# Kernel optimization log

Hardware: AMD Instinct MI355X
Metric: run time of the kernel (lower is better)

## Reference

```python
import jax, jax.numpy as jnp
import numpy as np

EPS = 1e-5


def gather_nodes(nodes, idx):
    # nodes: [B,N,C], idx: [B,N,K] -> [B,N,K,C]
    return jax.vmap(lambda n, e: n[e])(nodes, idx)


def layer_norm(x, g, b):
    m = jnp.mean(x, axis=-1, keepdims=True)
    v = jnp.mean((x - m) ** 2, axis=-1, keepdims=True)
    return (x - m) * jax.lax.rsqrt(v + EPS) * g + b


def linear(x, W, b):
    return x @ W + b


def setup_inputs() -> dict:
    key = jax.random.key(0)
    B, N, K, H = 2, 2048, 48, 128
    ks = jax.random.split(key, 32)
    it = iter(range(32))
    def nrm(shape, scale=0.05):
        return jax.random.normal(ks[next(it)], shape, dtype=jnp.float32) * scale
    inp = {
        "h_V": nrm((B, N, H), 1.0),
        "h_V_atom": nrm((B, N, H), 1.0),
        "h_E": nrm((B, N, K, H), 1.0),
        # message MLP 1: in = H + 2*(H+H) = 5H = 640
        "W1": nrm((5 * H, H)), "b1": jnp.zeros((H,), jnp.float32),
        "W2": nrm((H, H)), "b2": jnp.zeros((H,), jnp.float32),
        "W3": nrm((H, H)), "b3": jnp.zeros((H,), jnp.float32),
        # message MLP 2: in = H + (H+H) = 3H = 384
        "W11": nrm((3 * H, H)), "b11": jnp.zeros((H,), jnp.float32),
        "W12": nrm((H, H)), "b12": jnp.zeros((H,), jnp.float32),
        "W13": nrm((H, H)), "b13": jnp.zeros((H,), jnp.float32),
        # FFN
        "W_in": nrm((H, 4 * H)), "b_in": jnp.zeros((4 * H,), jnp.float32),
        "W_out": nrm((4 * H, H)), "b_out": jnp.zeros((H,), jnp.float32),
        # LayerNorms
        "g1": jnp.ones((H,), jnp.float32), "be1": jnp.zeros((H,), jnp.float32),
        "g2": jnp.ones((H,), jnp.float32), "be2": jnp.zeros((H,), jnp.float32),
        "g3": jnp.ones((H,), jnp.float32), "be3": jnp.zeros((H,), jnp.float32),
        "mask_V": jnp.ones((B, N), jnp.float32),
        "mask_attend": jnp.ones((B, N, K), jnp.float32),
        "E_idx": jax.random.randint(ks[next(it)], (B, N, K), 0, N),
    }
    return inp


def reference(h_V, h_V_atom, h_E, W1, b1, W2, b2, W3, b3, W11, b11, W12, b12,
              W13, b13, W_in, b_in, W_out, b_out, g1, be1, g2, be2, g3, be3,
              mask_V, mask_attend, E_idx):
    gelu = lambda x: jax.nn.gelu(x, approximate=False)
    SCALE = 30.0
    K = h_E.shape[-2]

    # --- node message ---
    h_EV = jnp.concatenate([
        jnp.broadcast_to(h_V[:, :, None, :], h_E.shape[:3] + (h_V.shape[-1],)),
        h_E, gather_nodes(h_V, E_idx),
        h_E, gather_nodes(h_V_atom, E_idx),
    ], axis=-1)  # [B,N,K,5H]
    h_message = linear(gelu(linear(gelu(linear(h_EV, W1, b1)), W2, b2)), W3, b3)
    h_message = mask_attend[..., None] * h_message
    dh = jnp.sum(h_message, axis=-2) / SCALE
    h_V = layer_norm(h_V + dh, g1, be1)

    # --- FFN ---
    dh = linear(gelu(linear(h_V, W_in, b_in)), W_out, b_out)
    h_V = layer_norm(h_V + dh, g2, be2)
    h_V = mask_V[..., None] * h_V

    # --- edge update ---
    h_EV2 = jnp.concatenate([
        jnp.broadcast_to(h_V[:, :, None, :], h_E.shape[:3] + (h_V.shape[-1],)),
        h_E, gather_nodes(h_V, E_idx),
    ], axis=-1)  # [B,N,K,3H]
    h_message = linear(gelu(linear(gelu(linear(h_EV2, W11, b11)), W12, b12)), W13, b13)
    h_E = layer_norm(h_E + h_message, g3, be3)
    return (h_V, h_E)
```

## Files before the change

### kernel.cpp

```cpp
#include <hip/hip_runtime.h>
#include <hip/hip_bf16.h>

#define H 128
#define NN 2048
#define BB 2
#define EPSF 1e-5f

typedef __bf16 bf16;
typedef bf16 bf16x8 __attribute__((ext_vector_type(8)));
typedef bf16 bf16x4 __attribute__((ext_vector_type(4)));
typedef float f32x4 __attribute__((ext_vector_type(4)));

#define U1_F     155648
#define U2_F     679936
#define HVMID_F  1204224
#define V2_F     1990656
#define V1_F     2252800
#define HVMID_B  3457024

__device__ __forceinline__ float gelu_f(float x) {
    float u = x * x;
    float p = __builtin_fmaf(u, 0.044715f, 1.0f);
    float w = x * p;
    float e = __builtin_amdgcn_exp2f(w * -2.3022083f);
    return x * __builtin_amdgcn_rcpf(1.0f + e);
}

#define MFMA16(a, b, c) __builtin_amdgcn_mfma_f32_16x16x32_bf16((a), (b), (c), 0, 0, 0)

#define GEMM_PIPE(U, A_EXPR, B0p, B1p, ACC)                                       \
    {                                                                             \
        bf16x8 bq0[3], bq1[3];                                                    \
        _Pragma("unroll")                                                         \
        for (int j = 0; j < 3 && j < (U); ++j) {                                  \
            bq0[j] = *(const bf16x8*)((B0p) + j * 32);                            \
            bq1[j] = *(const bf16x8*)((B1p) + j * 32);                            \
        }                                                                         \
        bf16x8 afc[3], afn[3];                                                    \
        _Pragma("unroll")                                                         \
        for (int rt = 0; rt < 3; ++rt) { const int u = 0; afc[rt] = (A_EXPR); }   \
        _Pragma("unroll")                                                         \
        for (int uu = 0; uu < (U); ++uu) {                                        \
            if (uu + 1 < (U)) {                                                   \
                _Pragma("unroll")                                                 \
                for (int rt = 0; rt < 3; ++rt) { const int u = uu + 1; afn[rt] = (A_EXPR); } \
            }                                                                     \
            __builtin_amdgcn_s_setprio(1);                                        \
            _Pragma("unroll")                                                     \
            for (int rt = 0; rt < 3; ++rt) {                                      \
                ACC[rt][0] = MFMA16(afc[rt], bq0[uu % 3], ACC[rt][0]);            \
                ACC[rt][1] = MFMA16(afc[rt], bq1[uu % 3], ACC[rt][1]);            \
            }                                                                     \
            __builtin_amdgcn_s_setprio(0);                                        \
            if (uu + 3 < (U)) {                                                   \
                bq0[uu % 3] = *(const bf16x8*)((B0p) + (uu + 3) * 32);            \
                bq1[uu % 3] = *(const bf16x8*)((B1p) + (uu + 3) * 32);            \
            }                                                                     \
            _Pragma("unroll")                                                     \
            for (int rt = 0; rt < 3; ++rt) afc[rt] = afn[rt];                     \
        }                                                                         \
    }

#define PACK_STORE(DST, ROW, PCOL, V0, V1)                                        \
    {                                                                             \
        union { bf16 h[2]; unsigned u; } pk_;                                     \
        pk_.h[0] = (V0); pk_.h[1] = (V1);                                         \
        *(unsigned*)&DST[ROW][PCOL] = pk_.u;                                      \
    }

__global__ void prep_weights(const float* __restrict__ W1, const float* __restrict__ W2,
                             const float* __restrict__ W3, const float* __restrict__ W11,
                             const float* __restrict__ W12, const float* __restrict__ W13,
                             const float* __restrict__ Win, const float* __restrict__ Wout,
                             bf16* __restrict__ ws)
{
    int i = blockIdx.x * 256 + threadIdx.x;
    float v;
    if (i < 65536) {
        int c = i >> 9, k = i & 511, s = k >> 7, k0 = k & 127;
        if (s == 0)      v = W1[k0 * H + c];
        else if (s == 1) v = W1[(128 + k0) * H + c] + W1[(384 + k0) * H + c];
        else if (s == 2) v = W1[(256 + k0) * H + c];
        else             v = W1[(512 + k0) * H + c];
    } else if (i < 81920)  { int j = i - 65536;  int c = j >> 7, p = j & 127;
                             int k = (p & ~31) + ((p & 1) << 4) + ((p & 31) >> 1);
                             v = W2[k * H + c]; }
    else if (i < 98304)    { int j = i - 81920;  int c = j >> 7, p = j & 127;
                             int k = (p & ~31) + ((p & 1) << 4) + ((p & 31) >> 1);
                             v = W3[k * H + c]; }
    else if (i < 147456)   { int j = i - 98304;  int c = j / 384, k = j - c * 384; v = W11[k * H + c]; }
    else if (i < 163840)   { int j = i - 147456; int c = j >> 7, p = j & 127;
                             int k = (p & ~31) + ((p & 1) << 4) + ((p & 31) >> 1);
                             v = W12[k * H + c]; }
    else if (i < 180224)   { int j = i - 163840; int c = j >> 7, p = j & 127;
                             int k = (p & ~31) + ((p & 1) << 4) + ((p & 31) >> 1);
                             v = W13[k * H + c]; }
    else if (i < 245760)   { int j = i - 180224; int jj = j >> 7, k = j & 127; v = Win[k * 512 + jj]; }
    else                   { int j = i - 245760; int c = j >> 9, k = j & 511; v = Wout[k * H + c]; }
    ws[i] = (bf16)v;
}

__global__ __launch_bounds__(512) void u1_kernel(
    const float* __restrict__ hV, const float* __restrict__ hVa,
    const float* __restrict__ b1, const bf16* __restrict__ ws, float* __restrict__ wsf)
{
    int n0 = blockIdx.x * 128;
    int t = threadIdx.x, w = t >> 6, l = t & 63, l16 = l & 15, lg = l >> 4;
    int wm = w >> 2, wn = w & 3;
    __shared__ __align__(16) bf16 sA[128][136];
    __shared__ __align__(16) bf16 sB[128][136];

    #pragma unroll
    for (int i = 0; i < 8; ++i) {
        int idx = t + i * 512;
        int row = idx >> 5, c4 = (idx & 31) << 2;
        f32x4 v = *(const f32x4*)(hV + (size_t)(n0 + row) * H + c4);
        bf16x4 o; o[0] = (bf16)v[0]; o[1] = (bf16)v[1]; o[2] = (bf16)v[2]; o[3] = (bf16)v[3];
        *(bf16x4*)(&sA[row][c4]) = o;
        f32x4 va = *(const f32x4*)(hVa + (size_t)(n0 + row) * H + c4);
        bf16x4 oa; oa[0] = (bf16)va[0]; oa[1] = (bf16)va[1]; oa[2] = (bf16)va[2]; oa[3] = (bf16)va[3];
        *(bf16x4*)(&sB[row][c4]) = oa;
    }
    __syncthreads();

    f32x4 accU[4][2], accV[4][2];
    #pragma unroll
    for (int rt = 0; rt < 4; ++rt)
        #pragma unroll
        for (int c2 = 0; c2 < 2; ++c2) {
            accU[rt][c2] = (f32x4){0.f, 0.f, 0.f, 0.f};
            accV[rt][c2] = (f32x4){0.f, 0.f, 0.f, 0.f};
        }
    #pragma unroll
    for (int kk = 0; kk < 4; ++kk) {
        bf16x8 af[4];
        #pragma unroll
        for (int rt = 0; rt < 4; ++rt)
            af[rt] = *(const bf16x8*)(&sA[wm * 64 + rt * 16 + l16][kk * 32 + lg * 8]);
        #pragma unroll
        for (int c2 = 0; c2 < 2; ++c2) {
            int c = wn * 32 + c2 * 16 + l16;
            bf16x8 bU = *(const bf16x8*)(&ws[(size_t)c * 512 + kk * 32 + lg * 8]);
            bf16x8 bV = *(const bf16x8*)(&ws[(size_t)c * 512 + 256 + kk * 32 + lg * 8]);
            #pragma unroll
            for (int rt = 0; rt < 4; ++rt) {
                accU[rt][c2] = MFMA16(af[rt], bU, accU[rt][c2]);
                accV[rt][c2] = MFMA16(af[rt], bV, accV[rt][c2]);
            }
        }
    }
    #pragma unroll
    for (int kk = 0; kk < 4; ++kk) {
        bf16x8 af[4];
        #pragma unroll
        for (int rt = 0; rt < 4; ++rt)
            af[rt] = *(const bf16x8*)(&sB[wm * 64 + rt * 16 + l16][kk * 32 + lg * 8]);
        #pragma unroll
        for (int c2 = 0; c2 < 2; ++c2) {
            int c = wn * 32 + c2 * 16 + l16;
            bf16x8 bV = *(const bf16x8*)(&ws[(size_t)c * 512 + 384 + kk * 32 + lg * 8]);
            #pragma unroll
            for (int rt = 0; rt < 4; ++rt)
                accV[rt][c2] = MFMA16(af[rt], bV, accV[rt][c2]);
        }
    }
    #pragma unroll
    for (int c2 = 0; c2 < 2; ++c2) {
        int col = wn * 32 + c2 * 16 + l16;
        float bb = b1[col];
        #pragma unroll
        for (int rt = 0; rt < 4; ++rt)
            #pragma unroll
            for (int i = 0; i < 4; ++i) {
                int row = wm * 64 + rt * 16 + lg * 4 + i;
                wsf[U1_F + (size_t)(n0 + row) * H + col] = accU[rt][c2][i] + bb;
                wsf[V1_F + (size_t)(n0 + row) * H + col] = accV[rt][c2][i];
            }
    }
}

__global__ __launch_bounds__(256, 4) void node_msg_kernel(
    const float* __restrict__ hV, const float* __restrict__ hE,
    const float* __restrict__ b2, const float* __restrict__ b3,
    const float* __restrict__ g1, const float* __restrict__ be1,
    const float* __restrict__ maskA, const int* __restrict__ Eidx,
    bf16* __restrict__ ws, float* __restrict__ wsf)
{
    __shared__ __align__(16) char smem[27136];
    bf16 (*sA)[136]  = (bf16(*)[136])smem;
    bf16 (*sH1)[136] = (bf16(*)[136])smem;
    bf16 (*sH2)[136] = (bf16(*)[136])(smem + 13056);
    float* sDH = (float*)(smem + 26112);

    int n = blockIdx.x, b = n >> 11;
    int t = threadIdx.x, w = t >> 6, l = t & 63, l16 = l & 15, lg = l >> 4;

    int col0 = w * 32 + l16, col1 = col0 + 16;
    int pcol = w * 32 + l16 * 2;
    float u1v0 = wsf[U1_F + (size_t)n * H + col0];
    float u1v1 = wsf[U1_F + (size_t)n * H + col1];
    float b2v0 = b2[col0], b2v1 = b2[col1];
    float b3v0 = b3[col0], b3v1 = b3[col1];

    float v1v0[3][4], v1v1[3][4];
    #pragma unroll
    for (int rt = 0; rt < 3; ++rt)
        #pragma unroll
        for (int i = 0; i < 4; ++i) {
            int row = rt * 16 + lg * 4 + i;
            int nbr = Eidx[n * 48 + row];
            const float* vp = wsf + V1_F + ((size_t)b * NN + nbr) * H;
            v1v0[rt][i] = vp[col0];
            v1v1[rt][i] = vp[col1];
        }

    #pragma unroll
    for (int i = 0; i < 6; ++i) {
        int idx = t + i * 256;
        int row = idx >> 5, c4 = (idx & 31) << 2;
        f32x4 v = *(const f32x4*)(hE + ((size_t)n * 48 + row) * H + c4);
        bf16x4 o; o[0] = (bf16)v[0]; o[1] = (bf16)v[1]; o[2] = (bf16)v[2]; o[3] = (bf16)v[3];
        *(bf16x4*)(&sA[row][c4]) = o;
    }
    __syncthreads();

    f32x4 acc[3][2];
    #pragma unroll
    for (int rt = 0; rt < 3; ++rt)
        #pragma unroll
        for (int c2 = 0; c2 < 2; ++c2) acc[rt][c2] = (f32x4){0.f, 0.f, 0.f, 0.f};
    {
        const bf16* B0 = ws + (size_t)col0 * 512 + 128 + lg * 8;
        const bf16* B1 = ws + (size_t)col1 * 512 + 128 + lg * 8;
        GEMM_PIPE(4, (*(const bf16x8*)(&sA[rt * 16 + l16][u * 32 + lg * 8])), B0, B1, acc)
    }
    __syncthreads();

    #pragma unroll
    for (int rt = 0; rt < 3; ++rt)
        #pragma unroll
        for (int i = 0; i < 4; ++i) {
            int row = rt * 16 + lg * 4 + i;
            bf16 v0 = (bf16)gelu_f(acc[rt][0][i] + u1v0 + v1v0[rt][i]);
            bf16 v1 = (bf16)gelu_f(acc[rt][1][i] + u1v1 + v1v1[rt][i]);
            PACK_STORE(sH1, row, pcol, v0, v1)
        }
    __syncthreads();

    f32x4 a2[3][2];
    #pragma unroll
    for (int rt = 0; rt < 3; ++rt)
        #pragma unroll
        for (int c2 = 0; c2 < 2; ++c2) a2[rt][c2] = (f32x4){0.f, 0.f, 0.f, 0.f};
    {
        const bf16* B0 = ws + 65536 + (size_t)col0 * 128 + lg * 8;
        const bf16* B1 = ws + 65536 + (size_t)col1 * 128 + lg * 8;
        GEMM_PIPE(4, (*(const bf16x8*)(&sH1[rt * 16 + l16][u * 32 + lg * 8])), B0, B1, a2)
    }
    #pragma unroll
    for (int rt = 0; rt < 3; ++rt)
        #pragma unroll
        for (int i = 0; i < 4; ++i) {
            int row = rt * 16 + lg * 4 + i;
            bf16 v0 = (bf16)gelu_f(a2[rt][0][i] + b2v0);
            bf16 v1 = (bf16)gelu_f(a2[rt][1][i] + b2v1);
            PACK_STORE(sH2, row, pcol, v0, v1)
        }
    __syncthreads();

    float mk[3][4];
    #pragma unroll
    for (int rt = 0; rt < 3; ++rt)
        #pragma unroll
        for (int i = 0; i < 4; ++i)
            mk[rt][i] = maskA[n * 48 + rt * 16 + lg * 4 + i];

    f32x4 a3[3][2];
    #pragma unroll
    for (int rt = 0; rt < 3; ++rt)
        #pragma unroll
        for (int c2 = 0; c2 < 2; ++c2) a3[rt][c2] = (f32x4){0.f, 0.f, 0.f, 0.f};
    {
        const bf16* B0 = ws + 81920 + (size_t)col0 * 128 + lg * 8;
        const bf16* B1 = ws + 81920 + (size_t)col1 * 128 + lg * 8;
        GEMM_PIPE(4, (*(const bf16x8*)(&sH2[rt * 16 + l16][u * 32 + lg * 8])), B0, B1, a3)
    }
    float r0s = 0.f, r1s = 0.f;
    #pragma unroll
    for (int rt = 0; rt < 3; ++rt)
        #pragma unroll
        for (int i = 0; i < 4; ++i) {
            r0s += (a3[rt][0][i] + b3v0) * mk[rt][i];
            r1s += (a3[rt][1][i] + b3v1) * mk[rt][i];
        }
    r0s += __shfl_xor(r0s, 16); r0s += __shfl_xor(r0s, 32);
    r1s += __shfl_xor(r1s, 16); r1s += __shfl_xor(r1s, 32);
    if (l < 16) { sDH[w * 32 + l] = r0s; sDH[w * 32 + 16 + l] = r1s; }
    __syncthreads();

    if (w == 0) {
        float x0 = hV[(size_t)n * H + l] + sDH[l] * (1.0f / 30.0f);
        float x1 = hV[(size_t)n * H + l + 64] + sDH[l + 64] * (1.0f / 30.0f);
        float s1 = x0 + x1, s2 = x0 * x0 + x1 * x1;
        #pragma unroll
        for (int off = 32; off; off >>= 1) { s1 += __shfl_xor(s1, off); s2 += __shfl_xor(s2, off); }
        float m = s1 * (1.f / 128.f);
        float rs = rsqrtf(s2 * (1.f / 128.f) - m * m + EPSF);
        float y0 = (x0 - m) * rs * g1[l] + be1[l];
        float y1 = (x1 - m) * rs * g1[l + 64] + be1[l + 64];
        wsf[HVMID_F + (size_t)n * H + l] = y0;
        wsf[HVMID_F + (size_t)n * H + l + 64] = y1;
        ws[HVMID_B + (size_t)n * H + l] = (bf16)y0;
        ws[HVMID_B + (size_t)n * H + l + 64] = (bf16)y1;
    }
}

__global__ __launch_bounds__(512) void ffn_kernel(
    const float* __restrict__ b_in, const float* __restrict__ b_out,
    const float* __restrict__ b11, const float* __restrict__ g2,
    const float* __restrict__ be2, const float* __restrict__ maskV,
    bf16* __restrict__ ws, float* __restrict__ wsf, float* __restrict__ outV)
{
    int n0 = blockIdx.x * 32;
    int t = threadIdx.x, w = t >> 6, l = t & 63, l16 = l & 15, lg = l >> 4;

    __shared__ __align__(16) char smem[8704 + 33280];
    bf16 (*sA)[136]  = (bf16(*)[136])(smem);
    bf16 (*sFF)[520] = (bf16(*)[520])(smem + 8704);
    float (*sX)[132] = (float(*)[132])(smem + 8704);

    {
        int row = t >> 4, c8 = (t & 15) << 3;
        *(bf16x8*)(&sA[row][c8]) = *(const bf16x8*)(ws + HVMID_B + (size_t)(n0 + row) * H + c8);
    }
    __syncthreads();

    f32x4 a1[2][4];
    #pragma unroll
    for (int rt = 0; rt < 2; ++rt)
        #pragma unroll
        for (int ct = 0; ct < 4; ++ct) a1[rt][ct] = (f32x4){0.f, 0.f, 0.f, 0.f};
    #pragma unroll
    for (int kk = 0; kk < 4; ++kk) {
        bf16x8 af[2];
        #pragma unroll
        for (int rt = 0; rt < 2; ++rt)
            af[rt] = *(const bf16x8*)(&sA[rt * 16 + l16][kk * 32 + lg * 8]);
        #pragma unroll
        for (int ct = 0; ct < 4; ++ct) {
            int c = w * 64 + ct * 16 + l16;
            bf16x8 bfr = *(const bf16x8*)(&ws[180224 + (size_t)c * 128 + kk * 32 + lg * 8]);
            #pragma unroll
            for (int rt = 0; rt < 2; ++rt)
                a1[rt][ct] = MFMA16(af[rt], bfr, a1[rt][ct]);
        }
    }
    #pragma unroll
    for (int ct = 0; ct < 4; ++ct) {
        int c = w * 64 + ct * 16 + l16;
        float bb = b_in[c];
        #pragma unroll
        for (int rt = 0; rt < 2; ++rt)
            #pragma unroll
            for (int i = 0; i < 4; ++i) {
                int row = rt * 16 + lg * 4 + i;
                sFF[row][c] = (bf16)gelu_f(a1[rt][ct][i] + bb);
            }
    }
    __syncthreads();

    f32x4 a2[2];
    a2[0] = (f32x4){0.f, 0.f, 0.f, 0.f}; a2[1] = (f32x4){0.f, 0.f, 0.f, 0.f};
    int cc = w * 16 + l16;
    #pragma unroll
    for (int kk = 0; kk < 16; ++kk) {
        bf16x8 af[2];
        #pragma unroll
        for (int rt = 0; rt < 2; ++rt)
            af[rt] = *(const bf16x8*)(&sFF[rt * 16 + l16][kk * 32 + lg * 8]);
        bf16x8 bfr = *(const bf16x8*)(&ws[245760 + (size_t)cc * 512 + kk * 32 + lg * 8]);
        #pragma unroll
        for (int rt = 0; rt < 2; ++rt)
            a2[rt] = MFMA16(af[rt], bfr, a2[rt]);
    }
    __syncthreads();
    {
        float bb = b_out[cc];
        #pragma unroll
        for (int rt = 0; rt < 2; ++rt)
            #pragma unroll
            for (int i = 0; i < 4; ++i) {
                int row = rt * 16 + lg * 4 + i;
                sX[row][cc] = a2[rt][i] + bb + wsf[HVMID_F + (size_t)(n0 + row) * H + cc];
            }
    }
    __syncthreads();

    if (t < 128) {
        int row = t >> 2, q = t & 3;
        float xr[32], s1 = 0.f, s2 = 0.f;
        #pragma unroll
        for (int j = 0; j < 32; ++j) {
            float x = sX[row][q * 32 + j];
            xr[j] = x; s1 += x; s2 += x * x;
        }
        s1 += __shfl_xor(s1, 1); s1 += __shfl_xor(s1, 2);
        s2 += __shfl_xor(s2, 1); s2 += __shfl_xor(s2, 2);
        float m = s1 * (1.f / 128.f);
        float vv = s2 * (1.f / 128.f) - m * m;
        float rs = rsqrtf(vv + EPSF);
        float mv = maskV[n0 + row];
        #pragma unroll
        for (int j = 0; j < 32; ++j) {
            int c = q * 32 + j;
            float y = ((xr[j] - m) * rs * g2[c] + be2[c]) * mv;
            outV[(size_t)(n0 + row) * H + c] = y;
            sA[row][c] = (bf16)y;
        }
    }
    __syncthreads();

    f32x4 a3[2], a4[2];
    a3[0] = (f32x4){0.f, 0.f, 0.f, 0.f}; a3[1] = (f32x4){0.f, 0.f, 0.f, 0.f};
    a4[0] = (f32x4){0.f, 0.f, 0.f, 0.f}; a4[1] = (f32x4){0.f, 0.f, 0.f, 0.f};
    #pragma unroll
    for (int kk = 0; kk < 4; ++kk) {
        bf16x8 af[2];
        #pragma unroll
        for (int rt = 0; rt < 2; ++rt)
            af[rt] = *(const bf16x8*)(&sA[rt * 16 + l16][kk * 32 + lg * 8]);
        bf16x8 bU = *(const bf16x8*)(&ws[98304 + (size_t)cc * 384 + kk * 32 + lg * 8]);
        bf16x8 bV = *(const bf16x8*)(&ws[98304 + (size_t)cc * 384 + 256 + kk * 32 + lg * 8]);
        #pragma unroll
        for (int rt = 0; rt < 2; ++rt) {
            a3[rt] = MFMA16(af[rt], bU, a3[rt]);
            a4[rt] = MFMA16(af[rt], bV, a4[rt]);
        }
    }
    {
        float bb = b11[cc];
        #pragma unroll
        for (int rt = 0; rt < 2; ++rt)
            #pragma unroll
            for (int i = 0; i < 4; ++i) {
                int row = rt * 16 + lg * 4 + i;
                wsf[U2_F + (size_t)(n0 + row) * H + cc] = a3[rt][i] + bb;
                wsf[V2_F + (size_t)(n0 + row) * H + cc] = a4[rt][i];
            }
    }
}

__global__ __launch_bounds__(256, 4) void edge_kernel(
    const float* __restrict__ hE, const float* __restrict__ b12,
    const float* __restrict__ b13, const float* __restrict__ g3,
    const float* __restrict__ be3, const int* __restrict__ Eidx,
    const bf16* __restrict__ ws, const float* __restrict__ wsf,
    float* __restrict__ outE)
{
    __shared__ __align__(16) char smem[26112];
    bf16 (*sA)[136]  = (bf16(*)[136])smem;
    bf16 (*sH1)[136] = (bf16(*)[136])smem;
    bf16 (*sH2)[136] = (bf16(*)[136])(smem + 13056);
    float (*sP1)[4]  = (float(*)[4])smem;
    float (*sP2)[4]  = (float(*)[4])(smem + 1024);

    int n = blockIdx.x, b = n >> 11;
    int t = threadIdx.x, w = t >> 6, l = t & 63, l16 = l & 15, lg = l >> 4;

    int col0 = w * 32 + l16, col1 = col0 + 16;
    int pcol = w * 32 + l16 * 2;
    float u2v0 = wsf[U2_F + (size_t)n * H + col0];
    float u2v1 = wsf[U2_F + (size_t)n * H + col1];
    float b12v0 = b12[col0], b12v1 = b12[col1];
    float b13v0 = b13[col0], b13v1 = b13[col1];
    float g3v0 = g3[col0], g3v1 = g3[col1];
    float be3v0 = be3[col0], be3v1 = be3[col1];

    float v2v0[3][4], v2v1[3][4];
    #pragma unroll
    for (int rt = 0; rt < 3; ++rt)
        #pragma unroll
        for (int i = 0; i < 4; ++i) {
            int row = rt * 16 + lg * 4 + i;
            int nbr = Eidx[n * 48 + row];
            const float* vp = wsf + V2_F + ((size_t)b * NN + nbr) * H;
            v2v0[rt][i] = vp[col0];
            v2v1[rt][i] = vp[col1];
        }

    #pragma unroll
    for (int i = 0; i < 6; ++i) {
        int idx = t + i * 256;
        int row = idx >> 5, c4 = (idx & 31) << 2;
        f32x4 v = *(const f32x4*)(hE + ((size_t)n * 48 + row) * H + c4);
        bf16x4 o; o[0] = (bf16)v[0]; o[1] = (bf16)v[1]; o[2] = (bf16)v[2]; o[3] = (bf16)v[3];
        *(bf16x4*)(&sA[row][c4]) = o;
    }
    __syncthreads();

    f32x4 acc[3][2];
    #pragma unroll
    for (int rt = 0; rt < 3; ++rt)
        #pragma unroll
        for (int c2 = 0; c2 < 2; ++c2) acc[rt][c2] = (f32x4){0.f, 0.f, 0.f, 0.f};
    {
        const bf16* B0 = ws + 98304 + (size_t)col0 * 384 + 128 + lg * 8;
        const bf16* B1 = ws + 98304 + (size_t)col1 * 384 + 128 + lg * 8;
        GEMM_PIPE(4, (*(const bf16x8*)(&sA[rt * 16 + l16][u * 32 + lg * 8])), B0, B1, acc)
    }

    float rv[3][2][4];
    #pragma unroll
    for (int rt = 0; rt < 3; ++rt)
        #pragma unroll
        for (int c2 = 0; c2 < 2; ++c2)
            #pragma unroll
            for (int i = 0; i < 4; ++i)
                rv[rt][c2][i] = (float)sA[rt * 16 + lg * 4 + i][c2 ? col1 : col0];
    __syncthreads();

    #pragma unroll
    for (int rt = 0; rt < 3; ++rt)
        #pragma unroll
        for (int i = 0; i < 4; ++i) {
            int row = rt * 16 + lg * 4 + i;
            bf16 v0 = (bf16)gelu_f(acc[rt][0][i] + u2v0 + v2v0[rt][i]);
            bf16 v1 = (bf16)gelu_f(acc[rt][1][i] + u2v1 + v2v1[rt][i]);
            PACK_STORE(sH1, row, pcol, v0, v1)
        }
    __syncthreads();

    f32x4 a2[3][2];
    #pragma unroll
    for (int rt = 0; rt < 3; ++rt)
        #pragma unroll
        for (int c2 = 0; c2 < 2; ++c2) a2[rt][c2] = (f32x4){0.f, 0.f, 0.f, 0.f};
    {
        const bf16* B0 = ws + 147456 + (size_t)col0 * 128 + lg * 8;
        const bf16* B1 = ws + 147456 + (size_t)col1 * 128 + lg * 8;
        GEMM_PIPE(4, (*(const bf16x8*)(&sH1[rt * 16 + l16][u * 32 + lg * 8])), B0, B1, a2)
    }
    #pragma unroll
    for (int rt = 0; rt < 3; ++rt)
        #pragma unroll
        for (int i = 0; i < 4; ++i) {
            int row = rt * 16 + lg * 4 + i;
            bf16 v0 = (bf16)gelu_f(a2[rt][0][i] + b12v0);
            bf16 v1 = (bf16)gelu_f(a2[rt][1][i] + b12v1);
            PACK_STORE(sH2, row, pcol, v0, v1)
        }
    __syncthreads();

    f32x4 a3[3][2];
    #pragma unroll
    for (int rt = 0; rt < 3; ++rt)
        #pragma unroll
        for (int c2 = 0; c2 < 2; ++c2) a3[rt][c2] = (f32x4){0.f, 0.f, 0.f, 0.f};
    {
        const bf16* B0 = ws + 163840 + (size_t)col0 * 128 + lg * 8;
        const bf16* B1 = ws + 163840 + (size_t)col1 * 128 + lg * 8;
        GEMM_PIPE(4, (*(const bf16x8*)(&sH2[rt * 16 + l16][u * 32 + lg * 8])), B0, B1, a3)
    }

    float s1r[3][4], s2r[3][4];
    #pragma unroll
    for (int rt = 0; rt < 3; ++rt)
        #pragma unroll
        for (int i = 0; i < 4; ++i) { s1r[rt][i] = 0.f; s2r[rt][i] = 0.f; }
    #pragma unroll
    for (int c2 = 0; c2 < 2; ++c2) {
        float bb = c2 ? b13v1 : b13v0;
        #pragma unroll
        for (int rt = 0; rt < 3; ++rt)
            #pragma unroll
            for (int i = 0; i < 4; ++i) {
                float v = a3[rt][c2][i] + bb + rv[rt][c2][i];
                a3[rt][c2][i] = v;
                s1r[rt][i] += v; s2r[rt][i] += v * v;
            }
    }
    #pragma unroll
    for (int mseg = 1; mseg < 16; mseg <<= 1)
        #pragma unroll
        for (int rt = 0; rt < 3; ++rt)
            #pragma unroll
            for (int i = 0; i < 4; ++i) {
                s1r[rt][i] += __shfl_xor(s1r[rt][i], mseg);
                s2r[rt][i] += __shfl_xor(s2r[rt][i], mseg);
            }
    if (l16 == 0) {
        #pragma unroll
        for (int rt = 0; rt < 3; ++rt)
            #pragma unroll
            for (int i = 0; i < 4; ++i) {
                int row = rt * 16 + lg * 4 + i;
                sP1[row][w] = s1r[rt][i];
                sP2[row][w] = s2r[rt][i];
            }
    }
    __syncthreads();

    #pragma unroll
    for (int rt = 0; rt < 3; ++rt)
        #pragma unroll
        for (int i = 0; i < 4; ++i) {
            int row = rt * 16 + lg * 4 + i;
            f32x4 p1 = *(const f32x4*)sP1[row];
            f32x4 p2 = *(const f32x4*)sP2[row];
            float s1 = p1[0] + p1[1] + p1[2] + p1[3];
            float s2 = p2[0] + p2[1] + p2[2] + p2[3];
            float mn = s1 * (1.f / 128.f);
            float rs = rsqrtf(s2 * (1.f / 128.f) - mn * mn + EPSF);
            size_t rb = ((size_t)n * 48 + row) * H;
            outE[rb + col0] = (a3[rt][0][i] - mn) * rs * g3v0 + be3v0;
            outE[rb + col1] = (a3[rt][1][i] - mn) * rs * g3v1 + be3v1;
        }
}

extern "C" void kernel_launch(void* const* d_in, const int* in_sizes, int n_in,
                              void* d_out, int out_size, void* d_ws, size_t ws_size,
                              hipStream_t stream)
{
    const float* hV    = (const float*)d_in[0];
    const float* hVa   = (const float*)d_in[1];
    const float* hE    = (const float*)d_in[2];
    const float* W1    = (const float*)d_in[3];
    const float* b1    = (const float*)d_in[4];
    const float* W2    = (const float*)d_in[5];
    const float* b2    = (const float*)d_in[6];
    const float* W3    = (const float*)d_in[7];
    const float* b3    = (const float*)d_in[8];
    const float* W11   = (const float*)d_in[9];
    const float* b11   = (const float*)d_in[10];
    const float* W12   = (const float*)d_in[11];
    const float* b12   = (const float*)d_in[12];
    const float* W13   = (const float*)d_in[13];
    const float* b13   = (const float*)d_in[14];
    const float* Win   = (const float*)d_in[15];
    const float* b_in  = (const float*)d_in[16];
    const float* Wout  = (const float*)d_in[17];
    const float* b_out = (const float*)d_in[18];
    const float* g1    = (const float*)d_in[19];
    const float* be1   = (const float*)d_in[20];
    const float* g2    = (const float*)d_in[21];
    const float* be2   = (const float*)d_in[22];
    const float* g3    = (const float*)d_in[23];
    const float* be3   = (const float*)d_in[24];
    const float* maskV = (const float*)d_in[25];
    const float* maskA = (const float*)d_in[26];
    const int*   Eidx  = (const int*)  d_in[27];

    bf16*  ws   = (bf16*)d_ws;
    float* wsf  = (float*)d_ws;
    float* outV = (float*)d_out;
    float* outE = outV + (size_t)BB * NN * H;

    prep_weights<<<1216, 256, 0, stream>>>(W1, W2, W3, W11, W12, W13, Win, Wout, ws);
    u1_kernel<<<32, 512, 0, stream>>>(hV, hVa, b1, ws, wsf);
    node_msg_kernel<<<BB * NN, 256, 0, stream>>>(hV, hE, b2, b3, g1, be1, maskA, Eidx, ws, wsf);
    ffn_kernel<<<BB * NN / 32, 512, 0, stream>>>(b_in, b_out, b11, g2, be2, maskV, ws, wsf, outV);
    edge_kernel<<<BB * NN, 256, 0, stream>>>(hE, b12, b13, g3, be3, Eidx, ws, wsf, outE);
}
```

Baseline: 174.5 us.

## Permute column layout of intermediates so gathers and residual reads use paired loads

```diff
diff --git a/kernel.cpp b/kernel.cpp
--- a/kernel.cpp
+++ b/kernel.cpp
@@ -10,6 +10,7 @@
 typedef bf16 bf16x8 __attribute__((ext_vector_type(8)));
 typedef bf16 bf16x4 __attribute__((ext_vector_type(4)));
 typedef float f32x4 __attribute__((ext_vector_type(4)));
+typedef float f32x2 __attribute__((ext_vector_type(2)));
 
 #define U1_F     155648
 #define U2_F     679936
@@ -79,7 +80,10 @@
     if (i < 65536) {
         int c = i >> 9, k = i & 511, s = k >> 7, k0 = k & 127;
         if (s == 0)      v = W1[k0 * H + c];
-        else if (s == 1) v = W1[(128 + k0) * H + c] + W1[(384 + k0) * H + c];
+        else if (s == 1) {
+            int klog = (k0 & ~31) + ((k0 & 1) << 4) + ((k0 & 31) >> 1);
+            v = W1[(128 + klog) * H + c] + W1[(384 + klog) * H + c];
+        }
         else if (s == 2) v = W1[(256 + k0) * H + c];
         else             v = W1[(512 + k0) * H + c];
     } else if (i < 81920)  { int j = i - 65536;  int c = j >> 7, p = j & 127;
@@ -88,7 +92,14 @@
     else if (i < 98304)    { int j = i - 81920;  int c = j >> 7, p = j & 127;
                              int k = (p & ~31) + ((p & 1) << 4) + ((p & 31) >> 1);
                              v = W3[k * H + c]; }
-    else if (i < 147456)   { int j = i - 98304;  int c = j / 384, k = j - c * 384; v = W11[k * H + c]; }
+    else if (i < 147456)   { int j = i - 98304;  int c = j / 384, k = j - c * 384;
+                             if (k >= 128 && k < 256) {
+                                 int p = k - 128;
+                                 int klog = (p & ~31) + ((p & 1) << 4) + ((p & 31) >> 1);
+                                 v = W11[(128 + klog) * H + c];
+                             } else {
+                                 v = W11[k * H + c];
+                             } }
     else if (i < 163840)   { int j = i - 147456; int c = j >> 7, p = j & 127;
                              int k = (p & ~31) + ((p & 1) << 4) + ((p & 31) >> 1);
                              v = W12[k * H + c]; }
@@ -164,17 +175,19 @@
                 accV[rt][c2] = MFMA16(af[rt], bV, accV[rt][c2]);
         }
     }
-    #pragma unroll
-    for (int c2 = 0; c2 < 2; ++c2) {
-        int col = wn * 32 + c2 * 16 + l16;
-        float bb = b1[col];
+    {
+        int col0 = wn * 32 + l16, col1 = col0 + 16;
+        int pcol = wn * 32 + l16 * 2;
+        float bb0 = b1[col0], bb1 = b1[col1];
         #pragma unroll
         for (int rt = 0; rt < 4; ++rt)
             #pragma unroll
             for (int i = 0; i < 4; ++i) {
                 int row = wm * 64 + rt * 16 + lg * 4 + i;
-                wsf[U1_F + (size_t)(n0 + row) * H + col] = accU[rt][c2][i] + bb;
-                wsf[V1_F + (size_t)(n0 + row) * H + col] = accV[rt][c2][i];
+                f32x2 su; su[0] = accU[rt][0][i] + bb0; su[1] = accU[rt][1][i] + bb1;
+                *(f32x2*)(wsf + U1_F + (size_t)(n0 + row) * H + pcol) = su;
+                f32x2 sv; sv[0] = accV[rt][0][i]; sv[1] = accV[rt][1][i];
+                *(f32x2*)(wsf + V1_F + (size_t)(n0 + row) * H + pcol) = sv;
             }
     }
 }
@@ -197,8 +210,7 @@
 
     int col0 = w * 32 + l16, col1 = col0 + 16;
     int pcol = w * 32 + l16 * 2;
-    float u1v0 = wsf[U1_F + (size_t)n * H + col0];
-    float u1v1 = wsf[U1_F + (size_t)n * H + col1];
+    f32x2 u1p = *(const f32x2*)(wsf + U1_F + (size_t)n * H + pcol);
     float b2v0 = b2[col0], b2v1 = b2[col1];
     float b3v0 = b3[col0], b3v1 = b3[col1];
 
@@ -209,18 +221,21 @@
         for (int i = 0; i < 4; ++i) {
             int row = rt * 16 + lg * 4 + i;
             int nbr = Eidx[n * 48 + row];
-            const float* vp = wsf + V1_F + ((size_t)b * NN + nbr) * H;
-            v1v0[rt][i] = vp[col0];
-            v1v1[rt][i] = vp[col1];
+            f32x2 vv = *(const f32x2*)(wsf + V1_F + ((size_t)b * NN + nbr) * H + pcol);
+            v1v0[rt][i] = vv[0];
+            v1v1[rt][i] = vv[1];
         }
 
     #pragma unroll
     for (int i = 0; i < 6; ++i) {
         int idx = t + i * 256;
-        int row = idx >> 5, c4 = (idx & 31) << 2;
-        f32x4 v = *(const f32x4*)(hE + ((size_t)n * 48 + row) * H + c4);
-        bf16x4 o; o[0] = (bf16)v[0]; o[1] = (bf16)v[1]; o[2] = (bf16)v[2]; o[3] = (bf16)v[3];
-        *(bf16x4*)(&sA[row][c4]) = o;
+        int row = idx >> 5, q = idx & 31;
+        int c0 = (q >> 3) * 32 + (q & 7) * 2;
+        const float* hp = hE + ((size_t)n * 48 + row) * H + c0;
+        f32x2 a = *(const f32x2*)(hp);
+        f32x2 c = *(const f32x2*)(hp + 16);
+        bf16x4 o; o[0] = (bf16)a[0]; o[1] = (bf16)c[0]; o[2] = (bf16)a[1]; o[3] = (bf16)c[1];
+        *(bf16x4*)(&sA[row][q * 4]) = o;
     }
     __syncthreads();
 
@@ -241,8 +256,8 @@
         #pragma unroll
         for (int i = 0; i < 4; ++i) {
             int row = rt * 16 + lg * 4 + i;
-            bf16 v0 = (bf16)gelu_f(acc[rt][0][i] + u1v0 + v1v0[rt][i]);
-            bf16 v1 = (bf16)gelu_f(acc[rt][1][i] + u1v1 + v1v1[rt][i]);
+            bf16 v0 = (bf16)gelu_f(acc[rt][0][i] + u1p[0] + v1v0[rt][i]);
+            bf16 v1 = (bf16)gelu_f(acc[rt][1][i] + u1p[1] + v1v1[rt][i]);
             PACK_STORE(sH1, row, pcol, v0, v1)
         }
     __syncthreads();
@@ -439,13 +454,14 @@
     }
     {
         float bb = b11[cc];
+        int pc = (cc & ~31) + l16 * 2 + ((cc >> 4) & 1);
         #pragma unroll
         for (int rt = 0; rt < 2; ++rt)
             #pragma unroll
             for (int i = 0; i < 4; ++i) {
                 int row = rt * 16 + lg * 4 + i;
-                wsf[U2_F + (size_t)(n0 + row) * H + cc] = a3[rt][i] + bb;
-                wsf[V2_F + (size_t)(n0 + row) * H + cc] = a4[rt][i];
+                wsf[U2_F + (size_t)(n0 + row) * H + pc] = a3[rt][i] + bb;
+                wsf[V2_F + (size_t)(n0 + row) * H + pc] = a4[rt][i];
             }
     }
 }
@@ -469,8 +485,7 @@
 
     int col0 = w * 32 + l16, col1 = col0 + 16;
     int pcol = w * 32 + l16 * 2;
-    float u2v0 = wsf[U2_F + (size_t)n * H + col0];
-    float u2v1 = wsf[U2_F + (size_t)n * H + col1];
+    f32x2 u2p = *(const f32x2*)(wsf + U2_F + (size_t)n * H + pcol);
     float b12v0 = b12[col0], b12v1 = b12[col1];
     float b13v0 = b13[col0], b13v1 = b13[col1];
     float g3v0 = g3[col0], g3v1 = g3[col1];
@@ -483,18 +498,21 @@
         for (int i = 0; i < 4; ++i) {
             int row = rt * 16 + lg * 4 + i;
             int nbr = Eidx[n * 48 + row];
-            const float* vp = wsf + V2_F + ((size_t)b * NN + nbr) * H;
-            v2v0[rt][i] = vp[col0];
-            v2v1[rt][i] = vp[col1];
+            f32x2 vv = *(const f32x2*)(wsf + V2_F + ((size_t)b * NN + nbr) * H + pcol);
+            v2v0[rt][i] = vv[0];
+            v2v1[rt][i] = vv[1];
         }
 
     #pragma unroll
     for (int i = 0; i < 6; ++i) {
         int idx = t + i * 256;
-        int row = idx >> 5, c4 = (idx & 31) << 2;
-        f32x4 v = *(const f32x4*)(hE + ((size_t)n * 48 + row) * H + c4);
-        bf16x4 o; o[0] = (bf16)v[0]; o[1] = (bf16)v[1]; o[2] = (bf16)v[2]; o[3] = (bf16)v[3];
-        *(bf16x4*)(&sA[row][c4]) = o;
+        int row = idx >> 5, q = idx & 31;
+        int c0 = (q >> 3) * 32 + (q & 7) * 2;
+        const float* hp = hE + ((size_t)n * 48 + row) * H + c0;
+        f32x2 a = *(const f32x2*)(hp);
+        f32x2 c = *(const f32x2*)(hp + 16);
+        bf16x4 o; o[0] = (bf16)a[0]; o[1] = (bf16)c[0]; o[2] = (bf16)a[1]; o[3] = (bf16)c[1];
+        *(bf16x4*)(&sA[row][q * 4]) = o;
     }
     __syncthreads();
 
@@ -509,14 +527,16 @@
         GEMM_PIPE(4, (*(const bf16x8*)(&sA[rt * 16 + l16][u * 32 + lg * 8])), B0, B1, acc)
     }
 
-    float rv[3][2][4];
-    #pragma unroll
-    for (int rt = 0; rt < 3; ++rt)
-        #pragma unroll
-        for (int c2 = 0; c2 < 2; ++c2)
-            #pragma unroll
-            for (int i = 0; i < 4; ++i)
-                rv[rt][c2][i] = (float)sA[rt * 16 + lg * 4 + i][c2 ? col1 : col0];
+    float rv0[3][4], rv1[3][4];
+    #pragma unroll
+    for (int rt = 0; rt < 3; ++rt)
+        #pragma unroll
+        for (int i = 0; i < 4; ++i) {
+            union { unsigned u; bf16 h[2]; } rp;
+            rp.u = *(const unsigned*)&sA[rt * 16 + lg * 4 + i][pcol];
+            rv0[rt][i] = (float)rp.h[0];
+            rv1[rt][i] = (float)rp.h[1];
+        }
     __syncthreads();
 
     #pragma unroll
@@ -524,8 +544,8 @@
         #pragma unroll
         for (int i = 0; i < 4; ++i) {
             int row = rt * 16 + lg * 4 + i;
-            bf16 v0 = (bf16)gelu_f(acc[rt][0][i] + u2v0 + v2v0[rt][i]);
-            bf16 v1 = (bf16)gelu_f(acc[rt][1][i] + u2v1 + v2v1[rt][i]);
+            bf16 v0 = (bf16)gelu_f(acc[rt][0][i] + u2p[0] + v2v0[rt][i]);
+            bf16 v1 = (bf16)gelu_f(acc[rt][1][i] + u2p[1] + v2v1[rt][i]);
             PACK_STORE(sH1, row, pcol, v0, v1)
         }
     __syncthreads();
@@ -568,17 +588,14 @@
         #pragma unroll
         for (int i = 0; i < 4; ++i) { s1r[rt][i] = 0.f; s2r[rt][i] = 0.f; }
     #pragma unroll
-    for (int c2 = 0; c2 < 2; ++c2) {
-        float bb = c2 ? b13v1 : b13v0;
-        #pragma unroll
-        for (int rt = 0; rt < 3; ++rt)
-            #pragma unroll
-            for (int i = 0; i < 4; ++i) {
-                float v = a3[rt][c2][i] + bb + rv[rt][c2][i];
-                a3[rt][c2][i] = v;
-                s1r[rt][i] += v; s2r[rt][i] += v * v;
-            }
-    }
+    for (int rt = 0; rt < 3; ++rt)
+        #pragma unroll
+        for (int i = 0; i < 4; ++i) {
+            float v0 = a3[rt][0][i] + b13v0 + rv0[rt][i];
+            float v1 = a3[rt][1][i] + b13v1 + rv1[rt][i];
+            a3[rt][0][i] = v0; a3[rt][1][i] = v1;
+            s1r[rt][i] = v0 + v1; s2r[rt][i] = v0 * v0 + v1 * v1;
+        }
     #pragma unroll
     for (int mseg = 1; mseg < 16; mseg <<= 1)
         #pragma unroll
```

After: 176.5 us (median of 2 runs). Within noise of the previous version (+1.2%).
